# Kernel tuning notes

Hardware: AMD Instinct MI355X
Metric: run time of the kernel (lower is better)

## Reference

```python
import jax, jax.numpy as jnp
import numpy as np


def setup_inputs() -> dict:
    key = jax.random.key(0)
    ks = jax.random.split(key, 6)
    B, Cin, H, W = 8, 512, 128, 128
    Ck, Cv, K = 256, 256, 64
    s = lambda fan: fan ** -0.5
    return {
        "x": jax.random.normal(ks[0], (B, Cin, H, W), jnp.float32),
        "context": jax.random.normal(ks[1], (B, Cv, K), jnp.float32),
        "Wq": jax.random.normal(ks[2], (Ck, Cin), jnp.float32) * s(Cin),
        "Wk": jax.random.normal(ks[3], (Ck, Cv), jnp.float32) * s(Cv),
        "Wv": jax.random.normal(ks[4], (Cv, Cv), jnp.float32) * s(Cv),
        "Wp": jax.random.normal(ks[5], (Cin, Cv), jnp.float32) * s(Cv),
    }


def reference(x, context, Wq, Wk, Wv, Wp):
    B, Cin, H, W = x.shape
    Ck = Wq.shape[0]
    scale = Ck ** -0.5
    xf = x.reshape(B, Cin, H * W)                      # [B, Cin, N]
    q = jnp.einsum("kc,bcn->bnk", Wq, xf)             # [B, N, Ck]
    k = jnp.einsum("kc,bcm->bkm", Wk, context)        # [B, Ck, K]
    v = jnp.einsum("vc,bcm->bmv", Wv, context)        # [B, K, Cv]
    sim = jnp.einsum("bnk,bkm->bnm", q, k) * scale    # [B, N, K]
    attn = jax.nn.softmax(sim, axis=-1)
    out = jnp.einsum("bnm,bmv->bnv", attn, v)         # [B, N, Cv]
    out = jnp.einsum("cv,bnv->bcn", Wp, out)          # [B, Cin, N]
    return out.reshape(B, Cin, H, W)
```

## Files before the change

### kernel.cpp

```cpp
#include <hip/hip_runtime.h>
#include <stdint.h>

#define B_    8
#define CIN   512
#define NPIX  16384
#define CK    256
#define KCTX  64
#define CV    256

typedef _Float16 f16;
typedef _Float16 f16x4 __attribute__((ext_vector_type(4)));
typedef _Float16 f16x8 __attribute__((ext_vector_type(8)));
typedef float    f32x4 __attribute__((ext_vector_type(4)));

#define LOG2E 1.44269504f

#define WQKT_OFF 0
#define WPV_OFF  524288

#define WAITVM(N) asm volatile("s_waitcnt vmcnt(" #N ")" ::: "memory")
#define LGKM0     asm volatile("s_waitcnt lgkmcnt(0)" ::: "memory")
#define SCHEDB    __builtin_amdgcn_sched_barrier(0)
#define SBAR      __builtin_amdgcn_s_barrier()

__device__ __forceinline__ void gl_lds16(const void* g, void* l) {
    __builtin_amdgcn_global_load_lds(
        (const __attribute__((address_space(1))) uint32_t*)g,
        (__attribute__((address_space(3))) uint32_t*)l, 16, 0, 0);
}

__global__ __launch_bounds__(1024) void prep(const float* __restrict__ ctx,
                                             const float* __restrict__ Wk,
                                             const float* __restrict__ Wv,
                                             const float* __restrict__ Wq,
                                             const float* __restrict__ Wp,
                                             char* __restrict__ ws) {
    __shared__ char lds[65536];
    char* ctx_t = lds;
    char* kv_s  = lds + 32768;

    const int p = blockIdx.x;
    const int b = blockIdx.y;
    const int path = p >> 1, h = p & 1;
    const int t = threadIdx.x;
    const int w = t >> 6, l = t & 63, g = l >> 4, ln = l & 15;

    {
        const int m4 = (t & 15) * 4, c4 = (t >> 4) * 4;
        const float* cp = ctx + (size_t)b * (CV * KCTX) + (size_t)c4 * KCTX + m4;
        f32x4 xr[4];
        #pragma unroll
        for (int i = 0; i < 4; ++i) xr[i] = *(const f32x4*)(cp + (size_t)i * KCTX);
        #pragma unroll
        for (int j = 0; j < 4; ++j) {
            f16x4 v4; v4[0] = (f16)xr[0][j]; v4[1] = (f16)xr[1][j]; v4[2] = (f16)xr[2][j]; v4[3] = (f16)xr[3][j];
            int m = m4 + j;
            *(f16x4*)(ctx_t + m * 512 + 16 * (((c4 >> 3) & 31) ^ (m & 7)) + 2 * (c4 & 7)) = v4;
        }
    }
    __syncthreads();

    {
        const float* W = path ? Wv : Wk;
        const int rbase = 64 * (w >> 2);
        const int mm = 16 * (w & 3) + ln;
        f32x4 acc[4] = {};
        for (int ks = 0; ks < 8; ++ks) {
            f16x8 bf = *(const f16x8*)(ctx_t + mm * 512 + 16 * ((4 * ks + g) ^ (mm & 7)));
            #pragma unroll
            for (int mi = 0; mi < 4; ++mi) {
                int row = rbase + 16 * mi + ln;
                const float* wp0 = W + (size_t)row * CV + 32 * ks + 8 * g;
                f32x4 lo = *(const f32x4*)wp0, hi = *(const f32x4*)(wp0 + 4);
                f16x8 af;
                #pragma unroll
                for (int j = 0; j < 4; ++j) { af[j] = (f16)lo[j]; af[4 + j] = (f16)hi[j]; }
                acc[mi] = __builtin_amdgcn_mfma_f32_16x16x32_f16(af, bf, acc[mi], 0, 0, 0);
            }
        }
        #pragma unroll
        for (int mi = 0; mi < 4; ++mi)
            #pragma unroll
            for (int r = 0; r < 4; ++r) {
                int row = rbase + 16 * mi + 4 * g + r;
                *(f16*)(kv_s + mm * 512 + 16 * ((((row >> 3) & 31)) ^ (mm & 7)) + 2 * (row & 7)) = (f16)acc[mi][r];
            }
    }
    __syncthreads();

    if (path == 0) {
        f32x4 acc2[4] = {};
        const int cA = 256 * h + 16 * w + ln;
        const float* qcol = Wq + cA;
        for (int ks = 0; ks < 8; ++ks) {
            f16x8 af;
            #pragma unroll
            for (int j = 0; j < 8; ++j)
                af[j] = (f16)qcol[(size_t)(32 * ks + 8 * g + j) * CIN];
            #pragma unroll
            for (int ni = 0; ni < 4; ++ni) {
                int m2 = 16 * ni + ln;
                f16x8 bf = *(const f16x8*)(kv_s + m2 * 512 + 16 * ((4 * ks + g) ^ (m2 & 7)));
                acc2[ni] = __builtin_amdgcn_mfma_f32_16x16x32_f16(af, bf, acc2[ni], 0, 0, 0);
            }
        }
        char* dst = ws + WQKT_OFF + b * 65536;
        #pragma unroll
        for (int ni = 0; ni < 4; ++ni)
            #pragma unroll
            for (int r = 0; r < 4; ++r) {
                int c = 256 * h + 16 * w + 4 * g + r, m2 = 16 * ni + ln;
                int byte = (c >> 6) * 8192 + m2 * 128 + 16 * (((c >> 3) & 7) ^ (m2 & 7)) + 2 * (c & 7);
                *(f16*)(dst + byte) = (f16)(acc2[ni][r] * 0.0625f);
            }
    } else {
        f32x4 acc2[4] = {};
        const int cA = 256 * h + 16 * w + ln;
        for (int ks = 0; ks < 8; ++ks) {
            const float* pp = Wp + (size_t)cA * CV + 32 * ks + 8 * g;
            f32x4 lo = *(const f32x4*)pp, hi = *(const f32x4*)(pp + 4);
            f16x8 af;
            #pragma unroll
            for (int j = 0; j < 4; ++j) { af[j] = (f16)lo[j]; af[4 + j] = (f16)hi[j]; }
            #pragma unroll
            for (int ni = 0; ni < 4; ++ni) {
                int m2 = 16 * ni + ln;
                f16x8 bf = *(const f16x8*)(kv_s + m2 * 512 + 16 * ((4 * ks + g) ^ (m2 & 7)));
                acc2[ni] = __builtin_amdgcn_mfma_f32_16x16x32_f16(af, bf, acc2[ni], 0, 0, 0);
            }
        }
        char* dst = ws + WPV_OFF + b * 65536;
        #pragma unroll
        for (int ni = 0; ni < 4; ++ni)
            #pragma unroll
            for (int r = 0; r < 4; ++r) {
                int c = 256 * h + 16 * w + 4 * g + r, m2 = 16 * ni + ln;
                int slot = (m2 >> 5) * 4 + ((m2 >> 2) & 3), jj = ((m2 >> 4) & 1) * 4 + (m2 & 3);
                *(f16*)(dst + c * 128 + 16 * (slot ^ (c & 7)) + 2 * jj) = (f16)acc2[ni][r];
            }
    }
}

__global__ __launch_bounds__(512, 4) void fused(const float* __restrict__ x,
                                                const char* __restrict__ ws,
                                                float* __restrict__ out) {
    __shared__ char lds[65536];
    char* x_s  = lds;
    char* wq_s = lds + 32768;

    const int b  = blockIdx.y;
    const int n0 = blockIdx.x * 128;
    const int t  = threadIdx.x;
    const int w  = t >> 6, l = t & 63, g = l >> 4, ln = l & 15;
    const int nB = 16 * w + ln;
    const int fnB = (nB ^ (nB >> 3)) & 7;

    const float* xb = x + (size_t)b * CIN * NPIX + n0;
    const char* wqkt_g = ws + WQKT_OFF + b * 65536;
    const char* wpv_g  = ws + WPV_OFF  + b * 65536;

    const int n4 = (t & 31) * 4;
    const int c4 = (t >> 5) * 4;
    const int cslot = (c4 >> 3) & 7;
    const int coff  = 2 * (c4 & 7);

    f32x4 xr[2][4];
    f32x4 accs[4] = {};

    gl_lds16(wqkt_g + t * 16, wq_s + t * 16);
    SCHEDB;
    {
        const float* xp = xb + (size_t)c4 * NPIX + n4;
        #pragma unroll
        for (int i = 0; i < 4; ++i) xr[0][i] = *(const f32x4*)(xp + (size_t)i * NPIX);
    }
    SCHEDB;
    {
        const float* xp = xb + (size_t)(64 + c4) * NPIX + n4;
        #pragma unroll
        for (int i = 0; i < 4; ++i) xr[1][i] = *(const f32x4*)(xp + (size_t)i * NPIX);
    }
    SCHEDB;
    WAITVM(4);
    SCHEDB;
    #pragma unroll
    for (int j = 0; j < 4; ++j) {
        f16x4 v4; v4[0] = (f16)xr[0][0][j]; v4[1] = (f16)xr[0][1][j]; v4[2] = (f16)xr[0][2][j]; v4[3] = (f16)xr[0][3][j];
        int n = n4 + j; int fn = (n ^ (n >> 3)) & 7;
        *(f16x4*)(x_s + n * 128 + 16 * (cslot ^ fn) + coff) = v4;
    }
    LGKM0; SCHEDB; SBAR; SCHEDB;

    #pragma unroll
    for (int s = 0; s < 8; ++s) {
        if (s > 0) {
            if (s == 7) { WAITVM(0); } else { WAITVM(4); }
            SCHEDB; SBAR; SCHEDB;
        }
        {
            const char* xc = x_s + (s & 1) * 16384;
            const char* wc = wq_s + (s & 1) * 8192;
            #pragma unroll
            for (int kk = 0; kk < 2; ++kk) {
                int kb = kk * 4 + g;
                f16x8 bf = *(const f16x8*)(xc + nB * 128 + 16 * (kb ^ fnB));
                #pragma unroll
                for (int mi = 0; mi < 4; ++mi) {
                    int mm = 16 * mi + ln;
                    f16x8 af = *(const f16x8*)(wc + mm * 128 + 16 * (kb ^ (mm & 7)));
                    accs[mi] = __builtin_amdgcn_mfma_f32_16x16x32_f16(af, bf, accs[mi], 0, 0, 0);
                }
            }
        }
        SCHEDB;
        if (s < 7) {
            gl_lds16(wqkt_g + (s + 1) * 8192 + t * 16, wq_s + ((s + 1) & 1) * 8192 + t * 16);
            SCHEDB;
        }
        if (s < 6) {
            const float* xp = xb + (size_t)((s + 2) * 64 + c4) * NPIX + n4;
            #pragma unroll
            for (int i = 0; i < 4; ++i) xr[s & 1][i] = *(const f32x4*)(xp + (size_t)i * NPIX);
            SCHEDB;
        }
        if (s < 7) {
            if (s < 6) { WAITVM(5); } else { WAITVM(1); }
            SCHEDB;
            char* xn = x_s + ((s + 1) & 1) * 16384;
            #pragma unroll
            for (int j = 0; j < 4; ++j) {
                f16x4 v4;
                v4[0] = (f16)xr[(s + 1) & 1][0][j]; v4[1] = (f16)xr[(s + 1) & 1][1][j];
                v4[2] = (f16)xr[(s + 1) & 1][2][j]; v4[3] = (f16)xr[(s + 1) & 1][3][j];
                int n = n4 + j; int fn = (n ^ (n >> 3)) & 7;
                *(f16x4*)(xn + n * 128 + 16 * (cslot ^ fn) + coff) = v4;
            }
        }
        LGKM0; SCHEDB; SBAR; SCHEDB;
    }

    #pragma unroll
    for (int r = 0; r < 8; ++r) {
        int ch = t + 512 * r;
        gl_lds16(wpv_g + ch * 16, lds + ch * 16);
    }

    float mx = accs[0][0];
    #pragma unroll
    for (int mi = 0; mi < 4; ++mi)
        #pragma unroll
        for (int r = 0; r < 4; ++r) mx = fmaxf(mx, accs[mi][r]);
    mx = fmaxf(mx, __shfl_xor(mx, 16, 64));
    mx = fmaxf(mx, __shfl_xor(mx, 32, 64));
    float pv[4][4];
    float sum = 0.f;
    #pragma unroll
    for (int mi = 0; mi < 4; ++mi)
        #pragma unroll
        for (int r = 0; r < 4; ++r) {
            float pe = __builtin_amdgcn_exp2f((accs[mi][r] - mx) * LOG2E);
            pv[mi][r] = pe; sum += pe;
        }
    sum += __shfl_xor(sum, 16, 64);
    sum += __shfl_xor(sum, 32, 64);
    float inv = 1.f / sum;

    f16x8 afr[2];
    #pragma unroll
    for (int kk = 0; kk < 2; ++kk)
        #pragma unroll
        for (int j = 0; j < 8; ++j)
            afr[kk][j] = (f16)(pv[2 * kk + (j >> 2)][j & 3] * inv);
    __syncthreads();

    float* ob = out + (size_t)b * CIN * NPIX + n0 + 16 * w + 4 * g;
    #pragma unroll 4
    for (int ct = 0; ct < 32; ++ct) {
        int c = 16 * ct + ln;
        f32x4 acc = {};
        #pragma unroll
        for (int kk = 0; kk < 2; ++kk) {
            f16x8 bf = *(const f16x8*)(lds + c * 128 + 16 * ((kk * 4 + g) ^ (c & 7)));
            acc = __builtin_amdgcn_mfma_f32_16x16x32_f16(afr[kk], bf, acc, 0, 0, 0);
        }
        *(f32x4*)(ob + (size_t)c * NPIX) = acc;
    }
}

extern "C" void kernel_launch(void* const* d_in, const int* in_sizes, int n_in,
                              void* d_out, int out_size, void* d_ws, size_t ws_size,
                              hipStream_t stream) {
    (void)in_sizes; (void)n_in; (void)out_size; (void)ws_size;
    const float* x   = (const float*)d_in[0];
    const float* ctx = (const float*)d_in[1];
    const float* Wq  = (const float*)d_in[2];
    const float* Wk  = (const float*)d_in[3];
    const float* Wv  = (const float*)d_in[4];
    const float* Wp  = (const float*)d_in[5];
    float* out = (float*)d_out;
    char* ws = (char*)d_ws;

    prep<<<dim3(4, B_), 1024, 0, stream>>>(ctx, Wk, Wv, Wq, Wp, ws);
    fused<<<dim3(NPIX / 128, B_), 512, 0, stream>>>(x, ws, out);
}
```

Before: 160.1 us.

## Drop LDS staging in fused kernel; read fragment-ordered weights directly from global

The prep kernel now writes the folded Wq·K and Wp·V matrices in MFMA-fragment order, so the fused kernel can load A/B operands straight from global/L2 memory with no LDS. The fused kernel also drops the double-buffered LDS pipeline, the barriers and the async global-to-LDS copies. x is loaded per thread with strided scalar loads and converted in registers. Blocks shrink to 256 threads covering 64 pixels. This removes barrier and LDS overhead and lets occupancy depend only on registers, at the cost of uncoalesced scalar x loads and redundant weight reads from cache in every wave.

```diff
diff --git a/kernel.cpp b/kernel.cpp
--- a/kernel.cpp
+++ b/kernel.cpp
@@ -15,19 +15,8 @@
 
 #define LOG2E 1.44269504f
 
-#define WQKT_OFF 0
-#define WPV_OFF  524288
-
-#define WAITVM(N) asm volatile("s_waitcnt vmcnt(" #N ")" ::: "memory")
-#define LGKM0     asm volatile("s_waitcnt lgkmcnt(0)" ::: "memory")
-#define SCHEDB    __builtin_amdgcn_sched_barrier(0)
-#define SBAR      __builtin_amdgcn_s_barrier()
-
-__device__ __forceinline__ void gl_lds16(const void* g, void* l) {
-    __builtin_amdgcn_global_load_lds(
-        (const __attribute__((address_space(1))) uint32_t*)g,
-        (__attribute__((address_space(3))) uint32_t*)l, 16, 0, 0);
-}
+#define WQK_OFF 0
+#define WPV_OFF 524288
 
 __global__ __launch_bounds__(1024) void prep(const float* __restrict__ ctx,
                                              const float* __restrict__ Wk,
@@ -104,13 +93,14 @@
                 acc2[ni] = __builtin_amdgcn_mfma_f32_16x16x32_f16(af, bf, acc2[ni], 0, 0, 0);
             }
         }
-        char* dst = ws + WQKT_OFF + b * 65536;
+        char* dst = ws + WQK_OFF + b * 65536;
         #pragma unroll
         for (int ni = 0; ni < 4; ++ni)
             #pragma unroll
             for (int r = 0; r < 4; ++r) {
-                int c = 256 * h + 16 * w + 4 * g + r, m2 = 16 * ni + ln;
-                int byte = (c >> 6) * 8192 + m2 * 128 + 16 * (((c >> 3) & 7) ^ (m2 & 7)) + 2 * (c & 7);
+                int c = 256 * h + 16 * w + 4 * g + r;
+                int s  = c >> 6, kk = (c >> 5) & 1, gk = (c >> 3) & 3, j = c & 7;
+                int byte = ((((s * 4 + ni) * 2 + kk) * 4 + gk) * 16 + ln) * 16 + 2 * j;
                 *(f16*)(dst + byte) = (f16)(acc2[ni][r] * 0.0625f);
             }
     } else {
@@ -131,118 +121,54 @@
         }
         char* dst = ws + WPV_OFF + b * 65536;
         #pragma unroll
-        for (int ni = 0; ni < 4; ++ni)
+        for (int ni = 0; ni < 4; ++ni) {
+            const int kkm = ni >> 1;
+            const int gm  = ln >> 2;
+            const int jm  = 4 * (ni & 1) + (ln & 3);
             #pragma unroll
             for (int r = 0; r < 4; ++r) {
-                int c = 256 * h + 16 * w + 4 * g + r, m2 = 16 * ni + ln;
-                int slot = (m2 >> 5) * 4 + ((m2 >> 2) & 3), jj = ((m2 >> 4) & 1) * 4 + (m2 & 3);
-                *(f16*)(dst + c * 128 + 16 * (slot ^ (c & 7)) + 2 * jj) = (f16)acc2[ni][r];
-            }
+                int c = 256 * h + 16 * w + 4 * g + r;
+                int ct = c >> 4, lnc = c & 15;
+                int byte = (((ct * 2 + kkm) * 4 + gm) * 16 + lnc) * 16 + 2 * jm;
+                *(f16*)(dst + byte) = (f16)acc2[ni][r];
+            }
+        }
     }
 }
 
-__global__ __launch_bounds__(512, 4) void fused(const float* __restrict__ x,
+__global__ __launch_bounds__(256, 3) void fused(const float* __restrict__ x,
                                                 const char* __restrict__ ws,
                                                 float* __restrict__ out) {
-    __shared__ char lds[65536];
-    char* x_s  = lds;
-    char* wq_s = lds + 32768;
-
     const int b  = blockIdx.y;
-    const int n0 = blockIdx.x * 128;
+    const int n0 = blockIdx.x * 64;
     const int t  = threadIdx.x;
     const int w  = t >> 6, l = t & 63, g = l >> 4, ln = l & 15;
-    const int nB = 16 * w + ln;
-    const int fnB = (nB ^ (nB >> 3)) & 7;
-
-    const float* xb = x + (size_t)b * CIN * NPIX + n0;
-    const char* wqkt_g = ws + WQKT_OFF + b * 65536;
-    const char* wpv_g  = ws + WPV_OFF  + b * 65536;
-
-    const int n4 = (t & 31) * 4;
-    const int c4 = (t >> 5) * 4;
-    const int cslot = (c4 >> 3) & 7;
-    const int coff  = 2 * (c4 & 7);
-
-    f32x4 xr[2][4];
+    const int nb = n0 + 16 * w;
+
+    const char* wqk = ws + WQK_OFF + b * 65536;
+    const char* wpv = ws + WPV_OFF + b * 65536;
+    const float* xg = x + (size_t)b * CIN * NPIX + (size_t)8 * g * NPIX + nb + ln;
+
     f32x4 accs[4] = {};
-
-    gl_lds16(wqkt_g + t * 16, wq_s + t * 16);
-    SCHEDB;
-    {
-        const float* xp = xb + (size_t)c4 * NPIX + n4;
-        #pragma unroll
-        for (int i = 0; i < 4; ++i) xr[0][i] = *(const f32x4*)(xp + (size_t)i * NPIX);
-    }
-    SCHEDB;
-    {
-        const float* xp = xb + (size_t)(64 + c4) * NPIX + n4;
-        #pragma unroll
-        for (int i = 0; i < 4; ++i) xr[1][i] = *(const f32x4*)(xp + (size_t)i * NPIX);
-    }
-    SCHEDB;
-    WAITVM(4);
-    SCHEDB;
-    #pragma unroll
-    for (int j = 0; j < 4; ++j) {
-        f16x4 v4; v4[0] = (f16)xr[0][0][j]; v4[1] = (f16)xr[0][1][j]; v4[2] = (f16)xr[0][2][j]; v4[3] = (f16)xr[0][3][j];
-        int n = n4 + j; int fn = (n ^ (n >> 3)) & 7;
-        *(f16x4*)(x_s + n * 128 + 16 * (cslot ^ fn) + coff) = v4;
-    }
-    LGKM0; SCHEDB; SBAR; SCHEDB;
-
-    #pragma unroll
+    #pragma unroll 2
     for (int s = 0; s < 8; ++s) {
-        if (s > 0) {
-            if (s == 7) { WAITVM(0); } else { WAITVM(4); }
-            SCHEDB; SBAR; SCHEDB;
-        }
-        {
-            const char* xc = x_s + (s & 1) * 16384;
-            const char* wc = wq_s + (s & 1) * 8192;
+        f16x8 bf[2];
+        #pragma unroll
+        for (int kk = 0; kk < 2; ++kk) {
+            const float* xp = xg + (size_t)(64 * s + 32 * kk) * NPIX;
+            float xv[8];
+            #pragma unroll
+            for (int j = 0; j < 8; ++j) xv[j] = xp[(size_t)j * NPIX];
+            #pragma unroll
+            for (int j = 0; j < 8; ++j) bf[kk][j] = (f16)xv[j];
+        }
+        #pragma unroll
+        for (int mi = 0; mi < 4; ++mi)
             #pragma unroll
             for (int kk = 0; kk < 2; ++kk) {
-                int kb = kk * 4 + g;
-                f16x8 bf = *(const f16x8*)(xc + nB * 128 + 16 * (kb ^ fnB));
-                #pragma unroll
-                for (int mi = 0; mi < 4; ++mi) {
-                    int mm = 16 * mi + ln;
-                    f16x8 af = *(const f16x8*)(wc + mm * 128 + 16 * (kb ^ (mm & 7)));
-                    accs[mi] = __builtin_amdgcn_mfma_f32_16x16x32_f16(af, bf, accs[mi], 0, 0, 0);
-                }
-            }
-        }
-        SCHEDB;
-        if (s < 7) {
-            gl_lds16(wqkt_g + (s + 1) * 8192 + t * 16, wq_s + ((s + 1) & 1) * 8192 + t * 16);
-            SCHEDB;
-        }
-        if (s < 6) {
-            const float* xp = xb + (size_t)((s + 2) * 64 + c4) * NPIX + n4;
-            #pragma unroll
-            for (int i = 0; i < 4; ++i) xr[s & 1][i] = *(const f32x4*)(xp + (size_t)i * NPIX);
-            SCHEDB;
-        }
-        if (s < 7) {
-            if (s < 6) { WAITVM(5); } else { WAITVM(1); }
-            SCHEDB;
-            char* xn = x_s + ((s + 1) & 1) * 16384;
-            #pragma unroll
-            for (int j = 0; j < 4; ++j) {
-                f16x4 v4;
-                v4[0] = (f16)xr[(s + 1) & 1][0][j]; v4[1] = (f16)xr[(s + 1) & 1][1][j];
-                v4[2] = (f16)xr[(s + 1) & 1][2][j]; v4[3] = (f16)xr[(s + 1) & 1][3][j];
-                int n = n4 + j; int fn = (n ^ (n >> 3)) & 7;
-                *(f16x4*)(xn + n * 128 + 16 * (cslot ^ fn) + coff) = v4;
-            }
-        }
-        LGKM0; SCHEDB; SBAR; SCHEDB;
-    }
-
-    #pragma unroll
-    for (int r = 0; r < 8; ++r) {
-        int ch = t + 512 * r;
-        gl_lds16(wpv_g + ch * 16, lds + ch * 16);
+                f16x8 af = *(const f16x8*)(wqk + ((((s * 4 + mi) * 2 + kk) * 4 + g) * 16 + ln) * 16);
+                accs[mi] = __builtin_amdgcn_mfma_f32_16x16x32_f16(af, bf[kk], accs[mi], 0, 0, 0);
+            }
     }
 
     float mx = accs[0][0];
@@ -271,17 +197,16 @@
         #pragma unroll
         for (int j = 0; j < 8; ++j)
             afr[kk][j] = (f16)(pv[2 * kk + (j >> 2)][j & 3] * inv);
-    __syncthreads();
-
-    float* ob = out + (size_t)b * CIN * NPIX + n0 + 16 * w + 4 * g;
+
+    float* ob = out + (size_t)b * CIN * NPIX + nb + 4 * g;
     #pragma unroll 4
     for (int ct = 0; ct < 32; ++ct) {
         int c = 16 * ct + ln;
         f32x4 acc = {};
         #pragma unroll
         for (int kk = 0; kk < 2; ++kk) {
-            f16x8 bf = *(const f16x8*)(lds + c * 128 + 16 * ((kk * 4 + g) ^ (c & 7)));
-            acc = __builtin_amdgcn_mfma_f32_16x16x32_f16(afr[kk], bf, acc, 0, 0, 0);
+            f16x8 bfp = *(const f16x8*)(wpv + (((ct * 2 + kk) * 4 + g) * 16 + ln) * 16);
+            acc = __builtin_amdgcn_mfma_f32_16x16x32_f16(afr[kk], bfp, acc, 0, 0, 0);
         }
         *(f32x4*)(ob + (size_t)c * NPIX) = acc;
     }
@@ -301,5 +226,5 @@
     char* ws = (char*)d_ws;
 
     prep<<<dim3(4, B_), 1024, 0, stream>>>(ctx, Wk, Wv, Wq, Wp, ws);
-    fused<<<dim3(NPIX / 128, B_), 512, 0, stream>>>(x, ws, out);
+    fused<<<dim3(NPIX / 64, B_), 256, 0, stream>>>(x, ws, out);
 }
```

New measurement: 220.1 us. +37.5%, slower.
